# Performance work log

Hardware: AMD Instinct MI355X
Metric: run time of the kernel (lower is better)

The kernel has to match this reference:

```python
import jax, jax.numpy as jnp
import numpy as np

SIGMA = 8.0          # self.sigama
IGNORE_THR = 0.5     # self.ignore_threshold

def _clog(p):
    # torch BCELoss clamps log at -100
    return jnp.clip(jnp.log(jnp.clip(p, 1e-12, 1.0)), -100.0, 0.0)

def _bce(p, t):
    return -(t * _clog(p) + (1.0 - t) * _clog(1.0 - p))

def _smooth_l1(a, b):
    d = jnp.abs(a - b)
    return jnp.where(d < 1.0, 0.5 * d * d, d - 0.5)

def setup_inputs() -> dict:
    key = jax.random.key(0)
    k1, k2, k3, k4, k5 = jax.random.split(key, 5)
    bs, T, C, H, W = 32, 50, 80, 76, 76
    inp = jax.random.normal(k1, (bs, 5 + C, H, W), dtype=jnp.float32) * 0.5
    cls = jax.random.randint(k2, (bs, T, 1), 0, C).astype(jnp.float32)
    xy = jax.random.uniform(k3, (bs, T, 2), minval=0.02, maxval=0.98)
    wh = jax.random.uniform(k4, (bs, T, 2), minval=0.02, maxval=0.30)
    targets = jnp.concatenate([cls, xy, wh], -1)
    # variable number of valid targets per image; zero rows are skipped by the loss
    nvalid = jax.random.randint(k5, (bs,), 5, T)
    tmask = (jnp.arange(T)[None, :] < nvalid[:, None]).astype(jnp.float32)
    targets = targets * tmask[..., None]
    return {"input": inp, "targets": targets}

def reference(input, targets):
    bs, A, H, W = input.shape
    C = A - 5
    T = targets.shape[1]
    dt = input.dtype

    pred = jnp.transpose(input, (0, 2, 3, 1))  # [bs,H,W,A]
    x = jax.nn.sigmoid(pred[..., 0])
    y = jax.nn.sigmoid(pred[..., 1])
    w = pred[..., 2]
    h = pred[..., 3]
    conf = jax.nn.sigmoid(pred[..., 4])
    pred_cls = jax.nn.sigmoid(pred[..., 5:])

    gx_grid = jnp.arange(W, dtype=dt)[None, None, :]
    gy_grid = jnp.arange(H, dtype=dt)[None, :, None]
    pred_boxes = jnp.stack([x + gx_grid, y + gy_grid,
                            jnp.exp(w) * SIGMA, jnp.exp(h) * SIGMA], -1)
    pb = jax.lax.stop_gradient(pred_boxes)  # .detach() in original

    # ---- vectorized get_target ----
    valid = jnp.sum(targets, -1) != 0                      # [bs,T]
    gx = targets[..., 1] * W
    gy = targets[..., 2] * H
    gw = targets[..., 3] * W
    gh = targets[..., 4] * H
    gi = jnp.clip(gx.astype(jnp.int32), 0, W - 1)
    gj = jnp.clip(gy.astype(jnp.int32), 0, H - 1)
    cells = gj * W + gi
    # duplicate-cell skip: a target is dropped if an earlier VALID target hit the same cell
    tri = jnp.tril(jnp.ones((T, T), bool), -1)             # [t, t'] true iff t' < t
    dup = jnp.any((cells[:, :, None] == cells[:, None, :]) & valid[:, None, :] & tri[None], -1)
    eff = valid & ~dup
    efff = eff.astype(dt)
    n_obj = jnp.sum(efff)

    # IoU of every effective gt box vs all grid pred boxes (center format)
    g = jnp.stack([gx, gy, gw, gh], -1)[:, :, None, :]      # [bs,T,1,4]
    p = pb.reshape(bs, 1, H * W, 4)                         # [bs,1,HW,4]
    gx1, gy1 = g[..., 0] - g[..., 2] / 2, g[..., 1] - g[..., 3] / 2
    gx2, gy2 = g[..., 0] + g[..., 2] / 2, g[..., 1] + g[..., 3] / 2
    px1, py1 = p[..., 0] - p[..., 2] / 2, p[..., 1] - p[..., 3] / 2
    px2, py2 = p[..., 0] + p[..., 2] / 2, p[..., 1] + p[..., 3] / 2
    iw = jnp.clip(jnp.minimum(gx2, px2) - jnp.maximum(gx1, px1), 0.0)
    ih = jnp.clip(jnp.minimum(gy2, py2) - jnp.maximum(gy1, py1), 0.0)
    inter = iw * ih
    iou = inter / (g[..., 2] * g[..., 3] + p[..., 2] * p[..., 3] - inter + 1e-16)
    iou = iou.reshape(bs, T, H, W)
    ignore = jnp.any((iou >= IGNORE_THR) & eff[:, :, None, None], 1)  # [bs,H,W]

    bidx = jnp.broadcast_to(jnp.arange(bs)[:, None], (bs, T))
    def scat(vals):
        return jnp.zeros((bs, H, W), dt).at[bidx, gj, gi].add(efff * vals)
    mask = scat(jnp.ones_like(efff))
    scales = scat(2.0 - targets[..., 3] * targets[..., 4])
    tx = scat(gx - gi.astype(dt))
    ty = scat(gy - gj.astype(dt))
    tw = scat(jnp.log(gw / SIGMA + 1e-16))
    th = scat(jnp.log(gh / SIGMA + 1e-16))
    cls_idx = jnp.clip(targets[..., 0].astype(jnp.int32), 0, C - 1)
    tcls = jnp.zeros((bs, H, W, C), dt).at[bidx, gj, gi, cls_idx].add(efff)
    noobj_mask = jnp.where(ignore | (mask > 0), 0.0, 1.0).astype(dt)

    # ---- losses (all lambdas are 1) ----
    loss_x = (mask * scales * _bce(x, tx)).sum() / n_obj
    loss_y = (mask * scales * _bce(y, ty)).sum() / n_obj
    loss_w = (mask * scales * _smooth_l1(w, tw)).sum() / n_obj
    loss_h = (mask * scales * _smooth_l1(h, th)).sum() / n_obj
    loss_conf = (_bce(conf * mask, mask).sum()
                 + 0.5 * _bce(noobj_mask * conf, jnp.zeros_like(conf)).sum()) / n_obj
    loss_tcls = jnp.where(jnp.sum(tcls) > 0,
                          (mask[..., None] * _bce(pred_cls, tcls)).sum() / n_obj,
                          jnp.zeros((), dt))
    loss = loss_x + loss_y + loss_w + loss_h + loss_conf + loss_tcls
    return (loss, loss_x, loss_y, loss_w, loss_h, loss_conf, loss_tcls)
```

## Files before the change

kernel.cpp:

```cpp
#include <hip/hip_runtime.h>
#include <math.h>

#define BS 32
#define NT 50
#define NC 80
#define H 76
#define W 76
#define HW (H*W)
#define NA (5+NC)
#define SIGMA 8.0f
#define YBLK 23
#define NBLK (BS*YBLK)

__device__ __forceinline__ float clog_(float p){
    p = fminf(fmaxf(p, 1e-12f), 1.0f);
    float l = logf(p);
    return fminf(fmaxf(l, -100.0f), 0.0f);
}

__device__ __forceinline__ float sigmoid_(float v){
    return 1.0f / (1.0f + expf(-v));
}

__global__ __launch_bounds__(256) void yolo_main(
    const float* __restrict__ input,
    const float* __restrict__ targets,
    float*       __restrict__ partials,
    int*         __restrict__ counts)
{
    const int b   = blockIdx.x;
    const int yb  = blockIdx.y;
    const int tid = threadIdx.x;
    const int bid = b * YBLK + yb;

    __shared__ float4 s_box[NT];
    __shared__ float  s_area[NT];
    __shared__ int    s_cellc[NT];
    __shared__ float4 s_rest[NT];
    __shared__ float2 s_sc[NT];
    __shared__ int    s_cell[NT];
    __shared__ unsigned char s_valid[NT];
    __shared__ int    s_count;

    if (tid == 0) s_count = 0;

    float cls=0.f, xx=0.f, yy=0.f, ww=0.f, hh=0.f;
    bool valid = false;
    int cell0 = 0;
    if (tid < NT){
        const float* p = targets + ((size_t)b*NT + tid)*5;
        cls = p[0]; xx = p[1]; yy = p[2]; ww = p[3]; hh = p[4];
        valid = ((cls + xx + yy + ww + hh) != 0.0f);
        float gx = xx * (float)W, gy = yy * (float)H;
        int gi = min(max((int)gx, 0), W-1);
        int gj = min(max((int)gy, 0), H-1);
        cell0 = gj*W + gi;
        s_cell[tid]  = cell0;
        s_valid[tid] = valid ? 1 : 0;
    }
    __syncthreads();
    if (tid < NT && valid){
        bool dup = false;
        for (int u = 0; u < tid; ++u)
            if (s_valid[u] && s_cell[u] == cell0) dup = true;
        if (!dup){
            int idx = atomicAdd(&s_count, 1);
            float gx = xx*(float)W, gy = yy*(float)H;
            float gw = ww*(float)W, gh = hh*(float)H;
            int gi = min(max((int)gx, 0), W-1);
            int gj = min(max((int)gy, 0), H-1);
            s_box[idx]  = make_float4(gx - gw*0.5f, gy - gh*0.5f,
                                      gx + gw*0.5f, gy + gh*0.5f);
            s_area[idx] = gw * gh;
            s_cellc[idx]= cell0;
            s_rest[idx] = make_float4(gx - (float)gi, gy - (float)gj,
                                      logf(gw/SIGMA + 1e-16f),
                                      logf(gh/SIGMA + 1e-16f));
            s_sc[idx]   = make_float2(2.0f - ww*hh,
                                      (float)min(max((int)cls, 0), NC-1));
        }
    }
    __syncthreads();
    const int nb = s_count;

    const int cell = yb * 256 + tid;
    float lx=0.f, ly=0.f, lw=0.f, lh=0.f, lc=0.f, lt=0.f;
    if (cell < HW){
        const float* base = input + (size_t)b*NA*HW + cell;
        float vx = base[0];
        float vy = base[HW];
        float vw = base[2*HW];
        float vh = base[3*HW];
        float vc = base[4*HW];
        float x    = sigmoid_(vx);
        float y    = sigmoid_(vy);
        float conf = sigmoid_(vc);
        int i = cell / W, j = cell - i*W;
        float pw = expf(vw) * SIGMA;
        float ph = expf(vh) * SIGMA;
        float px = x + (float)j;
        float py = y + (float)i;
        float px1 = px - pw*0.5f, px2 = px + pw*0.5f;
        float py1 = py - ph*0.5f, py2 = py + ph*0.5f;
        float parea = pw * ph;

        bool ignore = false;
        int myt = -1;
        for (int t = 0; t < nb; ++t){
            float4 bx = s_box[t];
            float garea = s_area[t];
            float iw = fminf(bx.z, px2) - fmaxf(bx.x, px1);
            float ih = fminf(bx.w, py2) - fmaxf(bx.y, py1);
            iw = fmaxf(iw, 0.f); ih = fmaxf(ih, 0.f);
            float inter = iw * ih;
            ignore = ignore || (inter >= 0.5f*(garea + parea - inter + 1e-16f));
            if (s_cellc[t] == cell) myt = t;
        }

        if (myt >= 0){
            float4 r = s_rest[myt];
            float2 sc = s_sc[myt];
            float scale = sc.x;
            lx = scale * (-(r.x*clog_(x) + (1.f-r.x)*clog_(1.f-x)));
            ly = scale * (-(r.y*clog_(y) + (1.f-r.y)*clog_(1.f-y)));
            float dw = fabsf(vw - r.z);
            lw = scale * (dw < 1.f ? 0.5f*dw*dw : dw - 0.5f);
            float dh = fabsf(vh - r.w);
            lh = scale * (dh < 1.f ? 0.5f*dh*dh : dh - 0.5f);
            lc = -clog_(conf);
            int cidx = (int)sc.y;
            const float* cb = base + 5*HW;
            float acc = 0.f;
            for (int c = 0; c < NC; ++c){
                float pc = sigmoid_(cb[(size_t)c*HW]);
                if (c == cidx) acc += -clog_(pc);
                else           acc += -clog_(1.f - pc);
            }
            lt = acc;
        } else if (!ignore){
            lc = 0.5f * (-clog_(1.0f - conf));
        }
    }

    #pragma unroll
    for (int off = 32; off > 0; off >>= 1){
        lx += __shfl_down(lx, off);
        ly += __shfl_down(ly, off);
        lw += __shfl_down(lw, off);
        lh += __shfl_down(lh, off);
        lc += __shfl_down(lc, off);
        lt += __shfl_down(lt, off);
    }
    __shared__ float s_red[4*6];
    if ((tid & 63) == 0){
        int wv = tid >> 6;
        s_red[wv*6+0] = lx; s_red[wv*6+1] = ly; s_red[wv*6+2] = lw;
        s_red[wv*6+3] = lh; s_red[wv*6+4] = lc; s_red[wv*6+5] = lt;
    }
    __syncthreads();
    if (tid < 6){
        float v = s_red[tid] + s_red[6+tid] + s_red[12+tid] + s_red[18+tid];
        partials[tid*NBLK + bid] = v;
    }
    if (yb == 0 && tid == 0) counts[b] = nb;
}

__global__ __launch_bounds__(256) void finalize_k(
    const float* __restrict__ partials,
    const int*   __restrict__ counts,
    float*       __restrict__ out)
{
    int tid = threadIdx.x;
    float loc[6] = {0,0,0,0,0,0};
    for (int k = tid; k < NBLK; k += 256){
        #pragma unroll
        for (int j = 0; j < 6; ++j) loc[j] += partials[j*NBLK + k];
    }
    float nloc = (tid < BS) ? (float)counts[tid] : 0.f;

    #pragma unroll
    for (int off = 32; off > 0; off >>= 1){
        #pragma unroll
        for (int j = 0; j < 6; ++j) loc[j] += __shfl_down(loc[j], off);
        nloc += __shfl_down(nloc, off);
    }
    __shared__ float s_red[4*7];
    if ((tid & 63) == 0){
        int wv = tid >> 6;
        #pragma unroll
        for (int j = 0; j < 6; ++j) s_red[wv*7+j] = loc[j];
        s_red[wv*7+6] = nloc;
    }
    __syncthreads();
    if (tid == 0){
        float s[7];
        #pragma unroll
        for (int j = 0; j < 7; ++j)
            s[j] = s_red[j] + s_red[7+j] + s_red[14+j] + s_red[21+j];
        float n = s[6];
        float inv = (n > 0.f) ? (1.0f / n) : 0.0f;
        float lx = s[0]*inv, ly = s[1]*inv, lw = s[2]*inv, lh = s[3]*inv;
        float lconf = s[4]*inv;
        float ltcls = (n > 0.f) ? s[5]*inv : 0.0f;
        out[0] = lx + ly + lw + lh + lconf + ltcls;
        out[1] = lx;
        out[2] = ly;
        out[3] = lw;
        out[4] = lh;
        out[5] = lconf;
        out[6] = ltcls;
    }
}

extern "C" void kernel_launch(void* const* d_in, const int* in_sizes, int n_in,
                              void* d_out, int out_size, void* d_ws, size_t ws_size,
                              hipStream_t stream) {
    const float* input   = (const float*)d_in[0];
    const float* targets = (const float*)d_in[1];
    float* out = (float*)d_out;

    float* partials = (float*)d_ws;
    int*   counts   = (int*)((char*)d_ws + 6*NBLK*sizeof(float));

    dim3 grid(BS, YBLK);
    yolo_main<<<grid, dim3(256), 0, stream>>>(input, targets, partials, counts);
    finalize_k<<<1, dim3(256), 0, stream>>>(partials, counts, out);
}
```

Measured before the change: 127.7 us.

## Fuse finalize into main kernel and parallelize class BCE across threads

Result: slower. 165.4 us (+29.6%).

```diff
diff --git a/kernel.cpp b/kernel.cpp
--- a/kernel.cpp
+++ b/kernel.cpp
@@ -22,11 +22,13 @@
     return 1.0f / (1.0f + expf(-v));
 }
 
-__global__ __launch_bounds__(256) void yolo_main(
-    const float* __restrict__ input,
-    const float* __restrict__ targets,
-    float*       __restrict__ partials,
-    int*         __restrict__ counts)
+__global__ __launch_bounds__(256) void yolo_fused(
+    const float*  __restrict__ input,
+    const float*  __restrict__ targets,
+    float*        __restrict__ partials,
+    int*          __restrict__ counts,
+    unsigned int* __restrict__ done,
+    float*        __restrict__ out)
 {
     const int b   = blockIdx.x;
     const int yb  = blockIdx.y;
@@ -34,7 +36,6 @@
     const int bid = b * YBLK + yb;
 
     __shared__ float4 s_box[NT];
-    __shared__ float  s_area[NT];
     __shared__ int    s_cellc[NT];
     __shared__ float4 s_rest[NT];
     __shared__ float2 s_sc[NT];
@@ -71,7 +72,6 @@
             int gj = min(max((int)gy, 0), H-1);
             s_box[idx]  = make_float4(gx - gw*0.5f, gy - gh*0.5f,
                                       gx + gw*0.5f, gy + gh*0.5f);
-            s_area[idx] = gw * gh;
             s_cellc[idx]= cell0;
             s_rest[idx] = make_float4(gx - (float)gi, gy - (float)gj,
                                       logf(gw/SIGMA + 1e-16f),
@@ -83,10 +83,23 @@
     __syncthreads();
     const int nb = s_count;
 
-    const int cell = yb * 256 + tid;
     float lx=0.f, ly=0.f, lw=0.f, lh=0.f, lc=0.f, lt=0.f;
+
+    const int cellLo = yb * 256;
+    const int cellHi = (cellLo + 256 < HW) ? cellLo + 256 : HW;
+    const float* binp = input + (size_t)b*NA*HW;
+    for (int t = 0; t < nb; ++t){
+        int q = s_cellc[t];
+        if (q >= cellLo && q < cellHi && tid < NC){
+            float pc = sigmoid_(binp[(size_t)(5+tid)*HW + q]);
+            int cidx = (int)s_sc[t].y;
+            lt += (tid == cidx) ? -clog_(pc) : -clog_(1.f - pc);
+        }
+    }
+
+    const int cell = cellLo + tid;
     if (cell < HW){
-        const float* base = input + (size_t)b*NA*HW + cell;
+        const float* base = binp + cell;
         float vx = base[0];
         float vy = base[HW];
         float vw = base[2*HW];
@@ -108,7 +121,7 @@
         int myt = -1;
         for (int t = 0; t < nb; ++t){
             float4 bx = s_box[t];
-            float garea = s_area[t];
+            float garea = (bx.z - bx.x) * (bx.w - bx.y);
             float iw = fminf(bx.z, px2) - fmaxf(bx.x, px1);
             float ih = fminf(bx.w, py2) - fmaxf(bx.y, py1);
             iw = fmaxf(iw, 0.f); ih = fmaxf(ih, 0.f);
@@ -119,8 +132,7 @@
 
         if (myt >= 0){
             float4 r = s_rest[myt];
-            float2 sc = s_sc[myt];
-            float scale = sc.x;
+            float scale = s_sc[myt].x;
             lx = scale * (-(r.x*clog_(x) + (1.f-r.x)*clog_(1.f-x)));
             ly = scale * (-(r.y*clog_(y) + (1.f-r.y)*clog_(1.f-y)));
             float dw = fabsf(vw - r.z);
@@ -128,15 +140,6 @@
             float dh = fabsf(vh - r.w);
             lh = scale * (dh < 1.f ? 0.5f*dh*dh : dh - 0.5f);
             lc = -clog_(conf);
-            int cidx = (int)sc.y;
-            const float* cb = base + 5*HW;
-            float acc = 0.f;
-            for (int c = 0; c < NC; ++c){
-                float pc = sigmoid_(cb[(size_t)c*HW]);
-                if (c == cidx) acc += -clog_(pc);
-                else           acc += -clog_(1.f - pc);
-            }
-            lt = acc;
         } else if (!ignore){
             lc = 0.5f * (-clog_(1.0f - conf));
         }
@@ -163,52 +166,52 @@
         partials[tid*NBLK + bid] = v;
     }
     if (yb == 0 && tid == 0) counts[b] = nb;
-}
-
-__global__ __launch_bounds__(256) void finalize_k(
-    const float* __restrict__ partials,
-    const int*   __restrict__ counts,
-    float*       __restrict__ out)
-{
-    int tid = threadIdx.x;
-    float loc[6] = {0,0,0,0,0,0};
-    for (int k = tid; k < NBLK; k += 256){
+
+    __shared__ unsigned s_last;
+    __threadfence();
+    if (tid == 0)
+        s_last = (atomicAdd(done, 1u) == (unsigned)(NBLK - 1)) ? 1u : 0u;
+    __syncthreads();
+    if (s_last){
+        __threadfence();
+        float loc[6] = {0,0,0,0,0,0};
+        for (int k = tid; k < NBLK; k += 256){
+            #pragma unroll
+            for (int jj = 0; jj < 6; ++jj) loc[jj] += partials[jj*NBLK + k];
+        }
+        float nloc = (tid < BS) ? (float)counts[tid] : 0.f;
         #pragma unroll
-        for (int j = 0; j < 6; ++j) loc[j] += partials[j*NBLK + k];
-    }
-    float nloc = (tid < BS) ? (float)counts[tid] : 0.f;
-
-    #pragma unroll
-    for (int off = 32; off > 0; off >>= 1){
-        #pragma unroll
-        for (int j = 0; j < 6; ++j) loc[j] += __shfl_down(loc[j], off);
-        nloc += __shfl_down(nloc, off);
-    }
-    __shared__ float s_red[4*7];
-    if ((tid & 63) == 0){
-        int wv = tid >> 6;
-        #pragma unroll
-        for (int j = 0; j < 6; ++j) s_red[wv*7+j] = loc[j];
-        s_red[wv*7+6] = nloc;
-    }
-    __syncthreads();
-    if (tid == 0){
-        float s[7];
-        #pragma unroll
-        for (int j = 0; j < 7; ++j)
-            s[j] = s_red[j] + s_red[7+j] + s_red[14+j] + s_red[21+j];
-        float n = s[6];
-        float inv = (n > 0.f) ? (1.0f / n) : 0.0f;
-        float lx = s[0]*inv, ly = s[1]*inv, lw = s[2]*inv, lh = s[3]*inv;
-        float lconf = s[4]*inv;
-        float ltcls = (n > 0.f) ? s[5]*inv : 0.0f;
-        out[0] = lx + ly + lw + lh + lconf + ltcls;
-        out[1] = lx;
-        out[2] = ly;
-        out[3] = lw;
-        out[4] = lh;
-        out[5] = lconf;
-        out[6] = ltcls;
+        for (int off = 32; off > 0; off >>= 1){
+            #pragma unroll
+            for (int jj = 0; jj < 6; ++jj) loc[jj] += __shfl_down(loc[jj], off);
+            nloc += __shfl_down(nloc, off);
+        }
+        __shared__ float s_fin[4*7];
+        if ((tid & 63) == 0){
+            int wv = tid >> 6;
+            #pragma unroll
+            for (int jj = 0; jj < 6; ++jj) s_fin[wv*7+jj] = loc[jj];
+            s_fin[wv*7+6] = nloc;
+        }
+        __syncthreads();
+        if (tid == 0){
+            float s[7];
+            #pragma unroll
+            for (int jj = 0; jj < 7; ++jj)
+                s[jj] = s_fin[jj] + s_fin[7+jj] + s_fin[14+jj] + s_fin[21+jj];
+            float n = s[6];
+            float inv = (n > 0.f) ? (1.0f / n) : 0.0f;
+            float lxo = s[0]*inv, lyo = s[1]*inv, lwo = s[2]*inv, lho = s[3]*inv;
+            float lconf = s[4]*inv;
+            float ltcls = (n > 0.f) ? s[5]*inv : 0.0f;
+            out[0] = lxo + lyo + lwo + lho + lconf + ltcls;
+            out[1] = lxo;
+            out[2] = lyo;
+            out[3] = lwo;
+            out[4] = lho;
+            out[5] = lconf;
+            out[6] = ltcls;
+        }
     }
 }
 
@@ -219,10 +222,12 @@
     const float* targets = (const float*)d_in[1];
     float* out = (float*)d_out;
 
-    float* partials = (float*)d_ws;
-    int*   counts   = (int*)((char*)d_ws + 6*NBLK*sizeof(float));
+    unsigned int* done    = (unsigned int*)d_ws;
+    float*        partials= (float*)((char*)d_ws + 64);
+    int*          counts  = (int*)((char*)d_ws + 64 + 6*NBLK*sizeof(float));
+
+    hipMemsetAsync(d_ws, 0, 64, stream);
 
     dim3 grid(BS, YBLK);
-    yolo_main<<<grid, dim3(256), 0, stream>>>(input, targets, partials, counts);
-    finalize_k<<<1, dim3(256), 0, stream>>>(partials, counts, out);
-}
+    yolo_fused<<<grid, dim3(256), 0, stream>>>(input, targets, partials, counts, done, out);
+}
```
